# Performance work log

Hardware: AMD Instinct MI355X
Metric: run time of the kernel (lower is better)

The kernel has to match this reference:

```python
import jax, jax.numpy as jnp
import numpy as np

DIM = 256
HEADS = 8
WS = 8
SHIFT = 0
MLP_HIDDEN = 1024
N = 16
HH = 64
WW = 64
EPS = 1e-6


def _rel_pos_index(ws):
    # same construction as the torch buffer
    coords = np.stack(np.meshgrid(np.arange(ws), np.arange(ws), indexing='ij'))  # [2,ws,ws]
    cf = coords.reshape(2, -1)  # [2, T]
    rel = cf[:, :, None] - cf[:, None, :]  # [2,T,T]
    rel = rel.transpose(1, 2, 0).copy()
    rel[:, :, 0] += ws - 1
    rel[:, :, 1] += ws - 1
    rel[:, :, 0] *= 2 * ws - 1
    return rel.sum(-1)  # [T,T] int


REL_IDX = jnp.asarray(_rel_pos_index(WS), dtype=jnp.int32)


def setup_inputs() -> dict:
    key = jax.random.key(0)
    ks = jax.random.split(key, 12)
    s = 0.02
    return {
        'x_seq': jax.random.normal(ks[0], (N, HH * WW, DIM), jnp.float32),
        'c': jax.random.normal(ks[1], (N, DIM), jnp.float32),
        'qkv_w': jax.random.normal(ks[2], (DIM, 3 * DIM), jnp.float32) * s,
        'qkv_b': jnp.zeros((3 * DIM,), jnp.float32),
        'proj_w': jax.random.normal(ks[3], (DIM, DIM), jnp.float32) * s,
        'proj_b': jnp.zeros((DIM,), jnp.float32),
        'rel_pos_bias': jax.random.normal(ks[4], ((2 * WS - 1) ** 2, HEADS), jnp.float32) * s,
        'ada_w': jax.random.normal(ks[5], (DIM, 6 * DIM), jnp.float32) * s,
        'ada_b': jnp.zeros((6 * DIM,), jnp.float32),
        'fc1_w': jax.random.normal(ks[6], (DIM, MLP_HIDDEN), jnp.float32) * s,
        'fc1_b': jnp.zeros((MLP_HIDDEN,), jnp.float32),
        'fc2_w': jax.random.normal(ks[7], (MLP_HIDDEN, DIM), jnp.float32) * s,
        'fc2_b': jnp.zeros((DIM,), jnp.float32),
        'H': HH,
        'W': WW,
    }


def _ln(x):
    mu = jnp.mean(x, axis=-1, keepdims=True)
    var = jnp.mean(jnp.square(x - mu), axis=-1, keepdims=True)
    return (x - mu) / jnp.sqrt(var + EPS)


def _modulate(x, shift, scale):
    return x * (1.0 + scale[:, None, :]) + shift[:, None, :]


def _window_attention(x, qkv_w, qkv_b, proj_w, proj_b, rel_pos_bias):
    B_, T, C = x.shape
    hd = C // HEADS
    qkv = (x @ qkv_w + qkv_b).reshape(B_, T, 3, HEADS, hd)
    q = qkv[:, :, 0].transpose(0, 2, 1, 3) * (hd ** -0.5)  # [B_,h,T,d]
    k = qkv[:, :, 1].transpose(0, 2, 1, 3)
    v = qkv[:, :, 2].transpose(0, 2, 1, 3)
    attn = jnp.einsum('bhtd,bhsd->bhts', q, k)
    bias = rel_pos_bias[REL_IDX.reshape(-1)].reshape(T, T, HEADS).transpose(2, 0, 1)  # [h,T,T]
    attn = jax.nn.softmax(attn + bias[None], axis=-1)
    out = jnp.einsum('bhts,bhsd->bhtd', attn, v)
    out = out.transpose(0, 2, 1, 3).reshape(B_, T, C)
    return out @ proj_w + proj_b


def reference(x_seq, c, qkv_w, qkv_b, proj_w, proj_b, rel_pos_bias,
              ada_w, ada_b, fc1_w, fc1_b, fc2_w, fc2_b, H, W):
    Nb, T, C = x_seq.shape
    ws = WS
    ada = jax.nn.silu(c) @ ada_w + ada_b  # [N, 6C]
    sh_msa, sc_msa, g_msa, sh_mlp, sc_mlp, g_mlp = jnp.split(ada, 6, axis=1)

    x = x_seq.reshape(Nb, H, W, C)
    pad_h = (ws - H % ws) % ws
    pad_w = (ws - W % ws) % ws
    if pad_h or pad_w:
        x = jnp.pad(x, ((0, 0), (0, pad_h), (0, pad_w), (0, 0)))
    Hp, Wp = x.shape[1], x.shape[2]
    if SHIFT > 0:
        x = jnp.roll(x, shift=(-SHIFT, -SHIFT), axis=(1, 2))

    # window partition: [N*nW, ws*ws, C]
    x_win = x.reshape(Nb, Hp // ws, ws, Wp // ws, ws, C).transpose(0, 1, 3, 2, 4, 5)
    x_win = x_win.reshape(-1, ws * ws, C)
    nW = (Hp // ws) * (Wp // ws)

    sh_w = jnp.repeat(sh_msa, nW, axis=0)
    sc_w = jnp.repeat(sc_msa, nW, axis=0)
    g_w = jnp.repeat(g_msa, nW, axis=0)

    h = _modulate(_ln(x_win), sh_w, sc_w)
    h = _window_attention(h, qkv_w, qkv_b, proj_w, proj_b, rel_pos_bias)
    x_win = x_win + g_w[:, None, :] * h

    # window unpartition
    x = x_win.reshape(Nb, Hp // ws, Wp // ws, ws, ws, C).transpose(0, 1, 3, 2, 4, 5)
    x = x.reshape(Nb, Hp, Wp, C)
    if SHIFT > 0:
        x = jnp.roll(x, shift=(SHIFT, SHIFT), axis=(1, 2))
    if pad_h or pad_w:
        x = x[:, :H, :W, :]
    x = x.reshape(Nb, T, C)

    h = _modulate(_ln(x), sh_mlp, sc_mlp)
    h = jax.nn.gelu(h @ fc1_w + fc1_b, approximate=True) @ fc2_w + fc2_b
    return x + g_mlp[:, None, :] * h
```

## Files before the change

kernel.cpp:

```cpp
#include <hip/hip_runtime.h>
#include <hip/hip_bf16.h>

#define TTOT 65536

using f32x4 = __attribute__((ext_vector_type(4))) float;
using s16x8 = __attribute__((ext_vector_type(8))) short;
typedef unsigned short u16;
using u16x8 = __attribute__((ext_vector_type(8))) u16;

typedef __attribute__((address_space(3))) void lds_void;
typedef __attribute__((address_space(1))) void g_void;

__device__ __forceinline__ float bf2f(u16 u) {
    union { unsigned int ui; float f; } v; v.ui = ((unsigned int)u) << 16; return v.f;
}

__device__ __forceinline__ u16 f2bf(float f) {
    return __bfloat16_as_ushort(__float2bfloat16(f));
}

__global__ void wconv_t(const float* __restrict__ w, __hip_bfloat16* __restrict__ wt,
                        int K, int N) {
    int idx = blockIdx.x * 256 + threadIdx.x;
    if (idx >= K * N) return;
    int n = idx / K, k = idx - n * K;
    wt[idx] = __float2bfloat16(w[(long)k * N + n]);
}

__global__ __launch_bounds__(256) void ada_kernel(const float* __restrict__ c,
                                                  const float* __restrict__ ada_w,
                                                  const float* __restrict__ ada_b,
                                                  float* __restrict__ ada) {
    __shared__ float sc[16 * 256];
    int tid = threadIdx.x;
    for (int i = tid; i < 16 * 256; i += 256) {
        float v = c[i];
        sc[i] = v / (1.0f + expf(-v));
    }
    __syncthreads();
    int j = blockIdx.x * 256 + tid;
    float b = ada_b[j];
    for (int n = 0; n < 16; n++) {
        float acc = b;
        for (int k = 0; k < 256; k++)
            acc += sc[n * 256 + k] * ada_w[(long)k * 1536 + j];
        ada[n * 1536 + j] = acc;
    }
}

__global__ __launch_bounds__(256) void ln_mod(const float* __restrict__ x,
                                              const float* __restrict__ ada,
                                              int off_sh, int off_sc,
                                              __hip_bfloat16* __restrict__ out) {
    int row = blockIdx.x * 4 + (threadIdx.x >> 6);
    int lane = threadIdx.x & 63;
    const float4 v = *(const float4*)&x[(long)row * 256 + lane * 4];
    float s = v.x + v.y + v.z + v.w;
    float s2 = v.x * v.x + v.y * v.y + v.z * v.z + v.w * v.w;
#pragma unroll
    for (int o = 32; o > 0; o >>= 1) {
        s += __shfl_xor(s, o, 64);
        s2 += __shfl_xor(s2, o, 64);
    }
    float mu = s * (1.0f / 256.0f);
    float var = s2 * (1.0f / 256.0f) - mu * mu;
    float rstd = rsqrtf(var + 1e-6f);
    int nb = row >> 12;
    const float* sh = &ada[nb * 1536 + off_sh];
    const float* scp = &ada[nb * 1536 + off_sc];
    float vv[4] = {v.x, v.y, v.z, v.w};
#pragma unroll
    for (int e = 0; e < 4; e++) {
        int col = lane * 4 + e;
        float val = (vv[e] - mu) * rstd;
        val = val * (1.0f + scp[col]) + sh[col];
        out[(long)row * 256 + col] = __float2bfloat16(val);
    }
}

template <int MODE>
__global__ __launch_bounds__(256) void gemm_bt(const __hip_bfloat16* __restrict__ A,
                                               const __hip_bfloat16* __restrict__ Bt,
                                               const float* __restrict__ bias,
                                               const float* __restrict__ resid,
                                               const float* __restrict__ ada,
                                               float* __restrict__ outf,
                                               __hip_bfloat16* __restrict__ outb,
                                               int M, int N, int K) {
    __shared__ u16 As[2][128 * 64];
    __shared__ u16 Bs[2][128 * 64];
    int tid = threadIdx.x;
    int lane = tid & 63;
    int wid = tid >> 6;
    int wr = wid >> 1, wc = wid & 1;
    int brow = blockIdx.y * 128;
    int bcol = blockIdx.x * 128;
    int la = lane & 15, lb = lane >> 4;

    f32x4 acc[4][4] = {};

    const u16* Ag = (const u16*)A;
    const u16* Bg = (const u16*)Bt;

    auto STAGE = [&](int k0, int buf) {
#pragma unroll
        for (int i = 0; i < 4; i++) {
            int c = (wid * 4 + i) * 64 + lane;
            int row = c >> 3;
            int sc = (c & 7) ^ (row & 7);
            __builtin_amdgcn_global_load_lds(
                (const g_void*)(Ag + (long)(brow + row) * K + k0 + sc * 8),
                (lds_void*)&As[buf][(wid * 4 + i) * 512], 16, 0, 0);
            __builtin_amdgcn_global_load_lds(
                (const g_void*)(Bg + (long)(bcol + row) * K + k0 + sc * 8),
                (lds_void*)&Bs[buf][(wid * 4 + i) * 512], 16, 0, 0);
        }
    };

    int NT = K >> 6;
    STAGE(0, 0);
    for (int t = 0; t < NT; ++t) {
        int cur = t & 1;
        if (t + 1 < NT) {
            STAGE((t + 1) << 6, cur ^ 1);
            asm volatile("s_waitcnt vmcnt(8)" ::: "memory");
        } else {
            asm volatile("s_waitcnt vmcnt(0)" ::: "memory");
        }
        __builtin_amdgcn_s_barrier();
#pragma unroll
        for (int kk8 = 0; kk8 < 8; kk8 += 4) {
            s16x8 af[4], bfr[4];
#pragma unroll
            for (int m = 0; m < 4; m++) {
                int R = wr * 64 + m * 16 + la;
                af[m] = *(const s16x8*)&As[cur][R * 64 + (((kk8 + lb) ^ (R & 7)) << 3)];
            }
#pragma unroll
            for (int n2 = 0; n2 < 4; n2++) {
                int R = wc * 64 + n2 * 16 + la;
                bfr[n2] = *(const s16x8*)&Bs[cur][R * 64 + (((kk8 + lb) ^ (R & 7)) << 3)];
            }
#pragma unroll
            for (int m = 0; m < 4; m++)
#pragma unroll
                for (int n2 = 0; n2 < 4; n2++)
                    acc[m][n2] = __builtin_amdgcn_mfma_f32_16x16x32_bf16(
                        af[m], bfr[n2], acc[m][n2], 0, 0, 0);
        }
        __builtin_amdgcn_s_barrier();
    }

    int nb = brow >> 12;
#pragma unroll
    for (int m = 0; m < 4; m++) {
#pragma unroll
        for (int n2 = 0; n2 < 4; n2++) {
#pragma unroll
            for (int r = 0; r < 4; r++) {
                int row = brow + wr * 64 + m * 16 + lb * 4 + r;
                int col = bcol + wc * 64 + n2 * 16 + la;
                float v = acc[m][n2][r] + bias[col];
                long oidx = (long)row * N + col;
                if (MODE == 0) {
                    outb[oidx] = __float2bfloat16(v);
                } else {
                    float g = ada[nb * 1536 + 512 + col];
                    outf[oidx] = resid[oidx] + g * v;
                }
            }
        }
    }
}

__global__ __launch_bounds__(256, 2) void mlp_fused(float* __restrict__ outf,
                                                    const __hip_bfloat16* __restrict__ fc1w,
                                                    const float* __restrict__ fc1_b,
                                                    const __hip_bfloat16* __restrict__ fc2w,
                                                    const float* __restrict__ fc2_b,
                                                    const float* __restrict__ ada) {
    __shared__ u16 xa[64 * 264];
    __shared__ u16 hb[64 * 264];

    int tid = threadIdx.x;
    int lane = tid & 63;
    int w = tid >> 6;
    int la = lane & 15, lb = lane >> 4;
    long mrow = (long)blockIdx.x * 64;
    int nb = (int)(mrow >> 12);

    const u16* F1 = (const u16*)fc1w;
    const u16* F2 = (const u16*)fc2w;

    const float* sh = &ada[nb * 1536 + 768];
    const float* scp = &ada[nb * 1536 + 1024];
#pragma unroll
    for (int i = 0; i < 16; i++) {
        int row = i * 4 + w;
        const float4 v = *(const float4*)&outf[(mrow + row) * 256 + lane * 4];
        float s = v.x + v.y + v.z + v.w;
        float s2 = v.x * v.x + v.y * v.y + v.z * v.z + v.w * v.w;
#pragma unroll
        for (int o = 32; o > 0; o >>= 1) {
            s += __shfl_xor(s, o, 64);
            s2 += __shfl_xor(s2, o, 64);
        }
        float mu = s * (1.0f / 256.0f);
        float var = s2 * (1.0f / 256.0f) - mu * mu;
        float rstd = rsqrtf(var + 1e-6f);
        float vv[4] = {v.x, v.y, v.z, v.w};
#pragma unroll
        for (int e = 0; e < 4; e++) {
            int col = lane * 4 + e;
            float val = (vv[e] - mu) * rstd;
            val = val * (1.0f + scp[col]) + sh[col];
            xa[row * 264 + col] = f2bf(val);
        }
    }
    __syncthreads();

    f32x4 acc2[4][4] = {};

#pragma unroll 1
    for (int c = 0; c < 4; c++) {
        f32x4 acc1[4][4] = {};
        const u16* B1 = F1 + (long)(c * 256 + w * 64) * 256;
        s16x8 bc[8];
#pragma unroll
        for (int ct = 0; ct < 4; ct++)
#pragma unroll
            for (int kk = 0; kk < 2; kk++)
                bc[ct * 2 + kk] = *(const s16x8*)&B1[(ct * 16 + la) * 256 + kk * 32 + lb * 8];
#pragma unroll
        for (int k0 = 0; k0 < 4; k0++) {
            s16x8 bn[8];
            if (k0 < 3) {
#pragma unroll
                for (int ct = 0; ct < 4; ct++)
#pragma unroll
                    for (int kk = 0; kk < 2; kk++)
                        bn[ct * 2 + kk] = *(const s16x8*)&B1[(ct * 16 + la) * 256 +
                                                             (k0 + 1) * 64 + kk * 32 + lb * 8];
            }
            s16x8 a[4][2];
#pragma unroll
            for (int rt = 0; rt < 4; rt++)
#pragma unroll
                for (int kk = 0; kk < 2; kk++)
                    a[rt][kk] = *(const s16x8*)&xa[(rt * 16 + la) * 264 +
                                                   k0 * 64 + kk * 32 + lb * 8];
#pragma unroll
            for (int kk = 0; kk < 2; kk++)
#pragma unroll
                for (int rt = 0; rt < 4; rt++)
#pragma unroll
                    for (int ct = 0; ct < 4; ct++)
                        acc1[rt][ct] = __builtin_amdgcn_mfma_f32_16x16x32_bf16(
                            a[rt][kk], bc[ct * 2 + kk], acc1[rt][ct], 0, 0, 0);
            if (k0 < 3) {
#pragma unroll
                for (int q = 0; q < 8; q++) bc[q] = bn[q];
            }
        }
#pragma unroll
        for (int ct = 0; ct < 4; ct++) {
            float b1v = fc1_b[c * 256 + w * 64 + ct * 16 + la];
#pragma unroll
            for (int rt = 0; rt < 4; rt++) {
#pragma unroll
                for (int r = 0; r < 4; r++) {
                    float v = acc1[rt][ct][r] + b1v;
                    float u2 = 1.5957691216057308f * (v + 0.044715f * v * v * v);
                    hb[(rt * 16 + lb * 4 + r) * 264 + w * 64 + ct * 16 + la] =
                        f2bf(v / (1.0f + __expf(-u2)));
                }
            }
        }
        __syncthreads();

        const u16* B2 = F2 + (long)(w * 64) * 1024 + c * 256;
        s16x8 bc2[8];
#pragma unroll
        for (int ct = 0; ct < 4; ct++)
#pragma unroll
            for (int kk = 0; kk < 2; kk++)
                bc2[ct * 2 + kk] = *(const s16x8*)&B2[(ct * 16 + la) * 1024 + kk * 32 + lb * 8];
#pragma unroll
        for (int k0 = 0; k0 < 4; k0++) {
            s16x8 bn2[8];
            if (k0 < 3) {
#pragma unroll
                for (int ct = 0; ct < 4; ct++)
#pragma unroll
                    for (int kk = 0; kk < 2; kk++)
                        bn2[ct * 2 + kk] = *(const s16x8*)&B2[(ct * 16 + la) * 1024 +
                                                              (k0 + 1) * 64 + kk * 32 + lb * 8];
            }
            s16x8 a[4][2];
#pragma unroll
            for (int rt = 0; rt < 4; rt++)
#pragma unroll
                for (int kk = 0; kk < 2; kk++)
                    a[rt][kk] = *(const s16x8*)&hb[(rt * 16 + la) * 264 +
                                                   k0 * 64 + kk * 32 + lb * 8];
#pragma unroll
            for (int kk = 0; kk < 2; kk++)
#pragma unroll
                for (int rt = 0; rt < 4; rt++)
#pragma unroll
                    for (int ct = 0; ct < 4; ct++)
                        acc2[rt][ct] = __builtin_amdgcn_mfma_f32_16x16x32_bf16(
                            a[rt][kk], bc2[ct * 2 + kk], acc2[rt][ct], 0, 0, 0);
            if (k0 < 3) {
#pragma unroll
                for (int q = 0; q < 8; q++) bc2[q] = bn2[q];
            }
        }
        __syncthreads();
    }

#pragma unroll
    for (int ct = 0; ct < 4; ct++) {
        int col = w * 64 + ct * 16 + la;
        float g = ada[nb * 1536 + 1280 + col];
        float b2v = fc2_b[col];
#pragma unroll
        for (int rt = 0; rt < 4; rt++) {
#pragma unroll
            for (int r = 0; r < 4; r++) {
                long row = mrow + rt * 16 + lb * 4 + r;
                long oidx = row * 256 + col;
                outf[oidx] = outf[oidx] + g * (acc2[rt][ct][r] + b2v);
            }
        }
    }
}

__global__ __launch_bounds__(256) void win_attn_mfma(const __hip_bfloat16* __restrict__ qkv,
                                                     const float* __restrict__ rpb,
                                                     __hip_bfloat16* __restrict__ out) {
    __shared__ float bias_s[64 * 64];
    __shared__ u16 vt[4][32 * 72];
    __shared__ u16 pl[4][64 * 72];

    int tid = threadIdx.x;
    int bid = blockIdx.x;
    int h = bid & 7;
    int w = tid >> 6;
    int lane = tid & 63;
    int la = lane & 15, lb = lane >> 4;
    int win = (bid >> 3) * 4 + w;
    int n = win >> 6;
    int wh = (win >> 3) & 7;
    int ww = win & 7;
    long base_row = (long)n * 4096 + (long)(wh * 8) * 64 + ww * 8;

    for (int i = tid; i < 4096; i += 256) {
        int t = i >> 6, j = i & 63;
        int idx = ((t >> 3) - (j >> 3) + 7) * 15 + ((t & 7) - (j & 7) + 7);
        bias_s[i] = rpb[idx * 8 + h];
    }

    const u16* qg = (const u16*)qkv;

    s16x8 qf[4], kf[4];
#pragma unroll
    for (int rt = 0; rt < 4; rt++) {
        int t = rt * 16 + la;
        long sr = base_row + (t >> 3) * 64 + (t & 7);
        qf[rt] = *(const s16x8*)(qg + sr * 768 + h * 32 + lb * 8);
        kf[rt] = *(const s16x8*)(qg + sr * 768 + 256 + h * 32 + lb * 8);
    }
#pragma unroll
    for (int g = 0; g < 4; g++) {
        int t = g * 16 + la;
        long sr = base_row + (t >> 3) * 64 + (t & 7);
        u16x8 vv = *(const u16x8*)(qg + sr * 768 + 512 + h * 32 + lb * 8);
#pragma unroll
        for (int e = 0; e < 8; e++) vt[w][(lb * 8 + e) * 72 + t] = vv[e];
    }

    f32x4 sa[4][4];
    f32x4 zero = {};
#pragma unroll
    for (int rt = 0; rt < 4; rt++)
#pragma unroll
        for (int ct = 0; ct < 4; ct++)
            sa[rt][ct] = __builtin_amdgcn_mfma_f32_16x16x32_bf16(qf[rt], kf[ct], zero, 0, 0, 0);

    __syncthreads();

    float rls[4][4];
#pragma unroll
    for (int rt = 0; rt < 4; rt++) {
#pragma unroll
        for (int r = 0; r < 4; r++) {
            int t = rt * 16 + lb * 4 + r;
            float v0 = sa[rt][0][r] * 0.17677669529663687f + bias_s[t * 64 + 0 * 16 + la];
            float v1 = sa[rt][1][r] * 0.17677669529663687f + bias_s[t * 64 + 1 * 16 + la];
            float v2 = sa[rt][2][r] * 0.17677669529663687f + bias_s[t * 64 + 2 * 16 + la];
            float v3 = sa[rt][3][r] * 0.17677669529663687f + bias_s[t * 64 + 3 * 16 + la];
            float mx = fmaxf(fmaxf(v0, v1), fmaxf(v2, v3));
#pragma unroll
            for (int o = 1; o < 16; o <<= 1) mx = fmaxf(mx, __shfl_xor(mx, o, 64));
            float p0 = __expf(v0 - mx), p1 = __expf(v1 - mx);
            float p2 = __expf(v2 - mx), p3 = __expf(v3 - mx);
            float sum = (p0 + p1) + (p2 + p3);
#pragma unroll
            for (int o = 1; o < 16; o <<= 1) sum += __shfl_xor(sum, o, 64);
            sa[rt][0][r] = p0; sa[rt][1][r] = p1; sa[rt][2][r] = p2; sa[rt][3][r] = p3;
            rls[rt][r] = 1.0f / sum;
        }
    }

#pragma unroll
    for (int rt = 0; rt < 4; rt++)
#pragma unroll
        for (int ct = 0; ct < 4; ct++)
#pragma unroll
            for (int r = 0; r < 4; r++)
                pl[w][(rt * 16 + lb * 4 + r) * 72 + ct * 16 + la] = f2bf(sa[rt][ct][r]);

    __syncthreads();

    f32x4 oa[4][2] = {};
#pragma unroll
    for (int ks = 0; ks < 2; ks++) {
        s16x8 vf[2];
#pragma unroll
        for (int dt = 0; dt < 2; dt++)
            vf[dt] = *(const s16x8*)&vt[w][(dt * 16 + la) * 72 + ks * 32 + lb * 8];
#pragma unroll
        for (int rt = 0; rt < 4; rt++) {
            s16x8 pf = *(const s16x8*)&pl[w][(rt * 16 + la) * 72 + ks * 32 + lb * 8];
#pragma unroll
            for (int dt = 0; dt < 2; dt++)
                oa[rt][dt] = __builtin_amdgcn_mfma_f32_16x16x32_bf16(pf, vf[dt], oa[rt][dt], 0, 0, 0);
        }
    }

#pragma unroll
    for (int rt = 0; rt < 4; rt++) {
#pragma unroll
        for (int r = 0; r < 4; r++) {
            int t = rt * 16 + lb * 4 + r;
            long sr = base_row + (t >> 3) * 64 + (t & 7);
#pragma unroll
            for (int dt = 0; dt < 2; dt++) {
                int d = dt * 16 + la;
                out[sr * 256 + h * 32 + d] = __float2bfloat16(oa[rt][dt][r] * rls[rt][r]);
            }
        }
    }
}

extern "C" void kernel_launch(void* const* d_in, const int* in_sizes, int n_in,
                              void* d_out, int out_size, void* d_ws, size_t ws_size,
                              hipStream_t stream) {
    const float* x_seq  = (const float*)d_in[0];
    const float* c      = (const float*)d_in[1];
    const float* qkv_w  = (const float*)d_in[2];
    const float* qkv_b  = (const float*)d_in[3];
    const float* proj_w = (const float*)d_in[4];
    const float* proj_b = (const float*)d_in[5];
    const float* rpb    = (const float*)d_in[6];
    const float* ada_w  = (const float*)d_in[7];
    const float* ada_b  = (const float*)d_in[8];
    const float* fc1_w  = (const float*)d_in[9];
    const float* fc1_b  = (const float*)d_in[10];
    const float* fc2_w  = (const float*)d_in[11];
    const float* fc2_b  = (const float*)d_in[12];

    char* ws = (char*)d_ws;
    float* ada             = (float*)ws;
    __hip_bfloat16* qkv_wt = (__hip_bfloat16*)(ws + 131072);
    __hip_bfloat16* proj_wt= (__hip_bfloat16*)(ws + 524288);
    __hip_bfloat16* fc1_wt = (__hip_bfloat16*)(ws + 655360);
    __hip_bfloat16* fc2_wt = (__hip_bfloat16*)(ws + 1179648);
    __hip_bfloat16* bufA   = (__hip_bfloat16*)(ws + 2097152);
    __hip_bfloat16* bufB   = (__hip_bfloat16*)(ws + 35651584);
    float* outf = (float*)d_out;

    wconv_t<<<(256 * 768 + 255) / 256, 256, 0, stream>>>(qkv_w, qkv_wt, 256, 768);
    wconv_t<<<(256 * 256 + 255) / 256, 256, 0, stream>>>(proj_w, proj_wt, 256, 256);
    wconv_t<<<(256 * 1024 + 255) / 256, 256, 0, stream>>>(fc1_w, fc1_wt, 256, 1024);
    wconv_t<<<(1024 * 256 + 255) / 256, 256, 0, stream>>>(fc2_w, fc2_wt, 1024, 256);

    ada_kernel<<<6, 256, 0, stream>>>(c, ada_w, ada_b, ada);

    ln_mod<<<TTOT / 4, 256, 0, stream>>>(x_seq, ada, 0, 256, bufA);

    {
        dim3 g(768 / 128, TTOT / 128);
        gemm_bt<0><<<g, 256, 0, stream>>>(bufA, qkv_wt, qkv_b, nullptr, ada,
                                          nullptr, bufB, TTOT, 768, 256);
    }
    win_attn_mfma<<<2048, 256, 0, stream>>>(bufB, rpb, bufA);

    {
        dim3 g(256 / 128, TTOT / 128);
        gemm_bt<1><<<g, 256, 0, stream>>>(bufA, proj_wt, proj_b, x_seq, ada,
                                          outf, nullptr, TTOT, 256, 256);
    }
    mlp_fused<<<TTOT / 64, 256, 0, stream>>>(outf, fc1_wt, fc1_b, fc2_wt, fc2_b, ada);
}
```

Before: 412.4 us.

## Make GEMMs multi-tile persistent and shrink MLP hidden chunk for occupancy

The QKV and projection GEMMs now have each block process several consecutive 128-row M tiles (4 and 2 respectively), with the K pipeline running continuously across tiles and the epilogue written out between them. This hides prologue load latency and cuts block count. The fused MLP now processes the hidden dimension in 8 chunks of 128 instead of 4 of 256. That halves the hidden LDS buffer and accumulator registers so occupancy can rise to 3 blocks per CU, at the cost of dropping the explicit register double-buffering of weight fragments and adding more barriers.

```diff
diff --git a/kernel.cpp b/kernel.cpp
--- a/kernel.cpp
+++ b/kernel.cpp
@@ -78,22 +78,23 @@
     }
 }
 
-template <int MODE>
-__global__ __launch_bounds__(256) void gemm_bt(const __hip_bfloat16* __restrict__ A,
+template <int MODE, int KM>
+__global__ __launch_bounds__(256) void gemm_ms(const __hip_bfloat16* __restrict__ A,
                                                const __hip_bfloat16* __restrict__ Bt,
                                                const float* __restrict__ bias,
                                                const float* __restrict__ resid,
                                                const float* __restrict__ ada,
                                                float* __restrict__ outf,
                                                __hip_bfloat16* __restrict__ outb,
-                                               int M, int N, int K) {
+                                               int N) {
+    constexpr int K = 256;
     __shared__ u16 As[2][128 * 64];
     __shared__ u16 Bs[2][128 * 64];
     int tid = threadIdx.x;
     int lane = tid & 63;
     int wid = tid >> 6;
     int wr = wid >> 1, wc = wid & 1;
-    int brow = blockIdx.y * 128;
+    long base = (long)blockIdx.y * (128 * KM);
     int bcol = blockIdx.x * 128;
     int la = lane & 15, lb = lane >> 4;
 
@@ -102,14 +103,14 @@
     const u16* Ag = (const u16*)A;
     const u16* Bg = (const u16*)Bt;
 
-    auto STAGE = [&](int k0, int buf) {
+    auto STAGE = [&](long brow, int k0, int buf) {
 #pragma unroll
         for (int i = 0; i < 4; i++) {
             int c = (wid * 4 + i) * 64 + lane;
             int row = c >> 3;
             int sc = (c & 7) ^ (row & 7);
             __builtin_amdgcn_global_load_lds(
-                (const g_void*)(Ag + (long)(brow + row) * K + k0 + sc * 8),
+                (const g_void*)(Ag + (brow + row) * K + k0 + sc * 8),
                 (lds_void*)&As[buf][(wid * 4 + i) * 512], 16, 0, 0);
             __builtin_amdgcn_global_load_lds(
                 (const g_void*)(Bg + (long)(bcol + row) * K + k0 + sc * 8),
@@ -117,12 +118,13 @@
         }
     };
 
-    int NT = K >> 6;
-    STAGE(0, 0);
-    for (int t = 0; t < NT; ++t) {
-        int cur = t & 1;
-        if (t + 1 < NT) {
-            STAGE((t + 1) << 6, cur ^ 1);
+    constexpr int NS = KM * 4;
+    STAGE(base, 0, 0);
+    for (int j = 0; j < NS; ++j) {
+        int cur = j & 1;
+        if (j + 1 < NS) {
+            int jm = j + 1;
+            STAGE(base + (long)(jm >> 2) * 128, (jm & 3) << 6, cur ^ 1);
             asm volatile("s_waitcnt vmcnt(8)" ::: "memory");
         } else {
             asm volatile("s_waitcnt vmcnt(0)" ::: "memory");
@@ -148,39 +150,43 @@
                     acc[m][n2] = __builtin_amdgcn_mfma_f32_16x16x32_bf16(
                         af[m], bfr[n2], acc[m][n2], 0, 0, 0);
         }
+
+        if ((j & 3) == 3) {
+            long brow = base + (long)(j >> 2) * 128;
+            int nb = (int)(brow >> 12);
+#pragma unroll
+            for (int m = 0; m < 4; m++) {
+#pragma unroll
+                for (int n2 = 0; n2 < 4; n2++) {
+#pragma unroll
+                    for (int r = 0; r < 4; r++) {
+                        long row = brow + wr * 64 + m * 16 + lb * 4 + r;
+                        int col = bcol + wc * 64 + n2 * 16 + la;
+                        float v = acc[m][n2][r] + bias[col];
+                        long oidx = row * N + col;
+                        if (MODE == 0) {
+                            outb[oidx] = __float2bfloat16(v);
+                        } else {
+                            float g = ada[nb * 1536 + 512 + col];
+                            outf[oidx] = resid[oidx] + g * v;
+                        }
+                        acc[m][n2][r] = 0.0f;
+                    }
+                }
+            }
+        }
         __builtin_amdgcn_s_barrier();
     }
-
-    int nb = brow >> 12;
-#pragma unroll
-    for (int m = 0; m < 4; m++) {
-#pragma unroll
-        for (int n2 = 0; n2 < 4; n2++) {
-#pragma unroll
-            for (int r = 0; r < 4; r++) {
-                int row = brow + wr * 64 + m * 16 + lb * 4 + r;
-                int col = bcol + wc * 64 + n2 * 16 + la;
-                float v = acc[m][n2][r] + bias[col];
-                long oidx = (long)row * N + col;
-                if (MODE == 0) {
-                    outb[oidx] = __float2bfloat16(v);
-                } else {
-                    float g = ada[nb * 1536 + 512 + col];
-                    outf[oidx] = resid[oidx] + g * v;
-                }
-            }
-        }
-    }
-}
-
-__global__ __launch_bounds__(256, 2) void mlp_fused(float* __restrict__ outf,
+}
+
+__global__ __launch_bounds__(256, 3) void mlp_fused(float* __restrict__ outf,
                                                     const __hip_bfloat16* __restrict__ fc1w,
                                                     const float* __restrict__ fc1_b,
                                                     const __hip_bfloat16* __restrict__ fc2w,
                                                     const float* __restrict__ fc2_b,
                                                     const float* __restrict__ ada) {
     __shared__ u16 xa[64 * 264];
-    __shared__ u16 hb[64 * 264];
+    __shared__ u16 hb[64 * 136];
 
     int tid = threadIdx.x;
     int lane = tid & 63;
@@ -222,98 +228,72 @@
     f32x4 acc2[4][4] = {};
 
 #pragma unroll 1
-    for (int c = 0; c < 4; c++) {
-        f32x4 acc1[4][4] = {};
-        const u16* B1 = F1 + (long)(c * 256 + w * 64) * 256;
-        s16x8 bc[8];
-#pragma unroll
-        for (int ct = 0; ct < 4; ct++)
-#pragma unroll
-            for (int kk = 0; kk < 2; kk++)
-                bc[ct * 2 + kk] = *(const s16x8*)&B1[(ct * 16 + la) * 256 + kk * 32 + lb * 8];
+    for (int c = 0; c < 8; c++) {
+        f32x4 acc1[4][2] = {};
+        const u16* B1 = F1 + (long)(c * 128 + w * 32) * 256;
 #pragma unroll
         for (int k0 = 0; k0 < 4; k0++) {
-            s16x8 bn[8];
-            if (k0 < 3) {
-#pragma unroll
-                for (int ct = 0; ct < 4; ct++)
-#pragma unroll
-                    for (int kk = 0; kk < 2; kk++)
-                        bn[ct * 2 + kk] = *(const s16x8*)&B1[(ct * 16 + la) * 256 +
-                                                             (k0 + 1) * 64 + kk * 32 + lb * 8];
-            }
-            s16x8 a[4][2];
-#pragma unroll
-            for (int rt = 0; rt < 4; rt++)
+            s16x8 b1r[2][2];
+#pragma unroll
+            for (int ct = 0; ct < 2; ct++)
 #pragma unroll
                 for (int kk = 0; kk < 2; kk++)
-                    a[rt][kk] = *(const s16x8*)&xa[(rt * 16 + la) * 264 +
-                                                   k0 * 64 + kk * 32 + lb * 8];
-#pragma unroll
-            for (int kk = 0; kk < 2; kk++)
+                    b1r[ct][kk] = *(const s16x8*)&B1[(ct * 16 + la) * 256 +
+                                                     k0 * 64 + kk * 32 + lb * 8];
+#pragma unroll
+            for (int kk = 0; kk < 2; kk++) {
+                s16x8 a[4];
 #pragma unroll
                 for (int rt = 0; rt < 4; rt++)
-#pragma unroll
-                    for (int ct = 0; ct < 4; ct++)
+                    a[rt] = *(const s16x8*)&xa[(rt * 16 + la) * 264 +
+                                               k0 * 64 + kk * 32 + lb * 8];
+#pragma unroll
+                for (int rt = 0; rt < 4; rt++)
+#pragma unroll
+                    for (int ct = 0; ct < 2; ct++)
                         acc1[rt][ct] = __builtin_amdgcn_mfma_f32_16x16x32_bf16(
-                            a[rt][kk], bc[ct * 2 + kk], acc1[rt][ct], 0, 0, 0);
-            if (k0 < 3) {
-#pragma unroll
-                for (int q = 0; q < 8; q++) bc[q] = bn[q];
-            }
-        }
-#pragma unroll
-        for (int ct = 0; ct < 4; ct++) {
-            float b1v = fc1_b[c * 256 + w * 64 + ct * 16 + la];
+                            a[rt], b1r[ct][kk], acc1[rt][ct], 0, 0, 0);
+            }
+        }
+#pragma unroll
+        for (int ct = 0; ct < 2; ct++) {
+            float b1v = fc1_b[c * 128 + w * 32 + ct * 16 + la];
 #pragma unroll
             for (int rt = 0; rt < 4; rt++) {
 #pragma unroll
                 for (int r = 0; r < 4; r++) {
                     float v = acc1[rt][ct][r] + b1v;
                     float u2 = 1.5957691216057308f * (v + 0.044715f * v * v * v);
-                    hb[(rt * 16 + lb * 4 + r) * 264 + w * 64 + ct * 16 + la] =
+                    hb[(rt * 16 + lb * 4 + r) * 136 + w * 32 + ct * 16 + la] =
                         f2bf(v / (1.0f + __expf(-u2)));
                 }
             }
         }
         __syncthreads();
 
-        const u16* B2 = F2 + (long)(w * 64) * 1024 + c * 256;
-        s16x8 bc2[8];
-#pragma unroll
-        for (int ct = 0; ct < 4; ct++)
-#pragma unroll
-            for (int kk = 0; kk < 2; kk++)
-                bc2[ct * 2 + kk] = *(const s16x8*)&B2[(ct * 16 + la) * 1024 + kk * 32 + lb * 8];
-#pragma unroll
-        for (int k0 = 0; k0 < 4; k0++) {
-            s16x8 bn2[8];
-            if (k0 < 3) {
-#pragma unroll
-                for (int ct = 0; ct < 4; ct++)
-#pragma unroll
-                    for (int kk = 0; kk < 2; kk++)
-                        bn2[ct * 2 + kk] = *(const s16x8*)&B2[(ct * 16 + la) * 1024 +
-                                                              (k0 + 1) * 64 + kk * 32 + lb * 8];
-            }
-            s16x8 a[4][2];
-#pragma unroll
-            for (int rt = 0; rt < 4; rt++)
+        const u16* B2 = F2 + (long)(w * 64) * 1024 + c * 128;
+#pragma unroll
+        for (int k0 = 0; k0 < 2; k0++) {
+            s16x8 b2r[4][2];
+#pragma unroll
+            for (int ct = 0; ct < 4; ct++)
 #pragma unroll
                 for (int kk = 0; kk < 2; kk++)
-                    a[rt][kk] = *(const s16x8*)&hb[(rt * 16 + la) * 264 +
-                                                   k0 * 64 + kk * 32 + lb * 8];
-#pragma unroll
-            for (int kk = 0; kk < 2; kk++)
+                    b2r[ct][kk] = *(const s16x8*)&B2[(ct * 16 + la) * 1024 +
+                                                     k0 * 64 + kk * 32 + lb * 8];
+#pragma unroll
+            for (int kk = 0; kk < 2; kk++) {
+                s16x8 a[4];
+#pragma unroll
+                for (int rt = 0; rt < 4; rt++)
+                    a[rt] = *(const s16x8*)&hb[(rt * 16 + la) * 136 +
+                                               k0 * 64 + kk * 32 + lb * 8];
 #pragma unroll
                 for (int rt = 0; rt < 4; rt++)
 #pragma unroll
                     for (int ct = 0; ct < 4; ct++)
                         acc2[rt][ct] = __builtin_amdgcn_mfma_f32_16x16x32_bf16(
-                            a[rt][kk], bc2[ct * 2 + kk], acc2[rt][ct], 0, 0, 0);
-            if (k0 < 3) {
-#pragma unroll
-                for (int q = 0; q < 8; q++) bc2[q] = bn2[q];
+                            a[rt], b2r[ct][kk], acc2[rt][ct], 0, 0, 0);
             }
         }
         __syncthreads();
@@ -491,16 +471,16 @@
     ln_mod<<<TTOT / 4, 256, 0, stream>>>(x_seq, ada, 0, 256, bufA);
 
     {
-        dim3 g(768 / 128, TTOT / 128);
-        gemm_bt<0><<<g, 256, 0, stream>>>(bufA, qkv_wt, qkv_b, nullptr, ada,
-                                          nullptr, bufB, TTOT, 768, 256);
+        dim3 g(768 / 128, TTOT / (128 * 4));
+        gemm_ms<0, 4><<<g, 256, 0, stream>>>(bufA, qkv_wt, qkv_b, nullptr, ada,
+                                             nullptr, bufB, 768);
     }
     win_attn_mfma<<<2048, 256, 0, stream>>>(bufB, rpb, bufA);
 
     {
-        dim3 g(256 / 128, TTOT / 128);
-        gemm_bt<1><<<g, 256, 0, stream>>>(bufA, proj_wt, proj_b, x_seq, ada,
-                                          outf, nullptr, TTOT, 256, 256);
+        dim3 g(256 / 128, TTOT / (128 * 2));
+        gemm_ms<1, 2><<<g, 256, 0, stream>>>(bufA, proj_wt, proj_b, x_seq, ada,
+                                             outf, nullptr, 256);
     }
     mlp_fused<<<TTOT / 64, 256, 0, stream>>>(outf, fc1_wt, fc1_b, fc2_wt, fc2_b, ada);
 }
```

Result: slower. 446.3 us (+8.2%).
